# Kernel tuning notes

Measured on AMD Instinct MI355X. Metric: run time of the kernel, lower is better.

Reference implementation:

```python
import jax, jax.numpy as jnp
import numpy as np

B, S, D, H = 4, 2048, 1024, 16
DQKV = max(1, D // H)  # 64


def setup_inputs() -> dict:
    key = jax.random.key(0)
    ks = jax.random.split(key, 12)
    std = 1.0 / np.sqrt(D)
    inp = {
        "query": jax.random.normal(ks[0], (B, S, D), dtype=jnp.float32),
        "key": jax.random.normal(ks[1], (B, S, D), dtype=jnp.float32),
        "value": jax.random.normal(ks[2], (B, S, D), dtype=jnp.float32),
        # per-head projection weights, stacked over heads: [H, DQKV, D] (torch Linear layout [out,in])
        "wq": jax.random.uniform(ks[3], (H, DQKV, D), jnp.float32, -std, std),
        "bq": jax.random.uniform(ks[4], (H, DQKV), jnp.float32, -std, std),
        "wk": jax.random.uniform(ks[5], (H, DQKV, D), jnp.float32, -std, std),
        "bk": jax.random.uniform(ks[6], (H, DQKV), jnp.float32, -std, std),
        "wv": jax.random.uniform(ks[7], (H, DQKV, D), jnp.float32, -std, std),
        "bv": jax.random.uniform(ks[8], (H, DQKV), jnp.float32, -std, std),
        # output projection: [D, H*DQKV]
        "wo": jax.random.uniform(ks[9], (D, H * DQKV), jnp.float32, -1.0 / np.sqrt(H * DQKV), 1.0 / np.sqrt(H * DQKV)),
        "bo": jax.random.uniform(ks[10], (D,), jnp.float32, -1.0 / np.sqrt(H * DQKV), 1.0 / np.sqrt(H * DQKV)),
    }
    return inp


def reference(query, key, value, wq, bq, wk, bk, wv, bv, wo, bo):
    # Per-head linear projections (batched over heads): [B, H, S, DQKV]
    Q = jnp.einsum("bsd,hed->bhse", query, wq) + bq[None, :, None, :]
    K = jnp.einsum("bsd,hed->bhse", key, wk) + bk[None, :, None, :]
    V = jnp.einsum("bsd,hed->bhse", value, wv) + bv[None, :, None, :]
    scale = jnp.asarray(DQKV, Q.dtype) ** 0.5
    # Full N x N attention scores per head (matches naive bmm+softmax+bmm)
    scores = jnp.einsum("bhse,bhte->bhst", Q, K) / scale
    attn = jax.nn.softmax(scores, axis=-1)
    ctx = jnp.einsum("bhst,bhte->bhse", attn, V)  # [B, H, S, DQKV]
    # Concat over heads in head-major order: [B, S, H*DQKV]
    concat = jnp.transpose(ctx, (0, 2, 1, 3)).reshape(ctx.shape[0], ctx.shape[2], H * DQKV)
    return jnp.einsum("bsf,df->bsd", concat, wo) + bo
```

## Files before the change

### kernel.cpp

```cpp
#include <hip/hip_runtime.h>
#include <stdint.h>
#include <stddef.h>


typedef __attribute__((ext_vector_type(8))) short short8;
typedef __attribute__((ext_vector_type(4))) float f32x4;

#if __has_builtin(__builtin_amdgcn_exp2f)
#define EXP2F __builtin_amdgcn_exp2f
#else
#define EXP2F exp2f
#endif
#if __has_builtin(__builtin_amdgcn_rcpf)
#define RCPF __builtin_amdgcn_rcpf
#else
#define RCPF(x) (1.0f / (x))
#endif

__device__ __forceinline__ uint16_t f2bf(float f) {
  uint32_t u = __builtin_bit_cast(uint32_t, f);
  u += 0x7FFFu + ((u >> 16) & 1u);
  return (uint16_t)(u >> 16);
}

__device__ __forceinline__ void gld16(const void* g, void* l) {
  __builtin_amdgcn_global_load_lds((const __attribute__((address_space(1))) void*)g,
                                   (__attribute__((address_space(3))) void*)l, 16, 0, 0);
}

__global__ __launch_bounds__(256) void cast3(const float* __restrict__ s0, const float* __restrict__ s1,
                                             const float* __restrict__ s2, uint16_t* __restrict__ d0,
                                             uint16_t* __restrict__ d1, uint16_t* __restrict__ d2,
                                             int n4) {
  const int z = blockIdx.y;
  const float* s = z == 0 ? s0 : (z == 1 ? s1 : s2);
  uint16_t* d = z == 0 ? d0 : (z == 1 ? d1 : d2);
  int i = blockIdx.x * 256 + threadIdx.x;
  if (i >= n4) return;
  float4 v = ((const float4*)s)[i];
  ushort4 o;
  o.x = f2bf(v.x); o.y = f2bf(v.y); o.z = f2bf(v.z); o.w = f2bf(v.w);
  ((ushort4*)d)[i] = o;
}

__global__ __launch_bounds__(256) void cast4(const float* __restrict__ s0, const float* __restrict__ s1,
                                             const float* __restrict__ s2, const float* __restrict__ s3,
                                             uint16_t* __restrict__ d0, uint16_t* __restrict__ d1,
                                             uint16_t* __restrict__ d2, uint16_t* __restrict__ d3,
                                             int n4) {
  const int z = blockIdx.y;
  const float* s = z == 0 ? s0 : (z == 1 ? s1 : (z == 2 ? s2 : s3));
  uint16_t* d = z == 0 ? d0 : (z == 1 ? d1 : (z == 2 ? d2 : d3));
  int i = blockIdx.x * 256 + threadIdx.x;
  if (i >= n4) return;
  float4 v = ((const float4*)s)[i];
  ushort4 o;
  o.x = f2bf(v.x); o.y = f2bf(v.y); o.z = f2bf(v.z); o.w = f2bf(v.w);
  ((ushort4*)d)[i] = o;
}

__device__ __forceinline__ void gemm_core(const uint16_t* __restrict__ A,
                                          const uint16_t* __restrict__ Bw,
                                          uint16_t* As, uint16_t* Bs,
                                          f32x4 acc[4][4], int m0, int n0) {
  constexpr int K = 1024;
  const int tid = threadIdx.x;
  const int w = tid >> 6, l = tid & 63;
  const int ln = l & 15, quad = l >> 4;
  const int wm = (w >> 1) * 64, wn = (w & 1) * 64;

  const uint16_t* Ag[2];
  const uint16_t* Bg[2];
  int lofs[2];
#pragma unroll
  for (int c = 0; c < 2; ++c) {
    int chunk = w * 128 + c * 64 + l;
    int r = chunk >> 2, cc = chunk & 3;
    Ag[c] = A + (size_t)(m0 + r) * K + cc * 8;
    Bg[c] = Bw + (size_t)(n0 + r) * K + cc * 8;
    lofs[c] = (w * 128 + c * 64) * 8;
  }

  for (int k0 = 0; k0 < K; k0 += 32) {
    __syncthreads();
#pragma unroll
    for (int c = 0; c < 2; ++c) {
      gld16(Ag[c] + k0, As + lofs[c]);
      gld16(Bg[c] + k0, Bs + lofs[c]);
    }
    __syncthreads();
    short8 a[4], b[4];
#pragma unroll
    for (int mt = 0; mt < 4; ++mt)
      a[mt] = *(const short8*)(As + (wm + mt * 16 + ln) * 32 + quad * 8);
#pragma unroll
    for (int nt = 0; nt < 4; ++nt)
      b[nt] = *(const short8*)(Bs + (wn + nt * 16 + ln) * 32 + quad * 8);
#pragma unroll
    for (int mt = 0; mt < 4; ++mt)
#pragma unroll
      for (int nt = 0; nt < 4; ++nt)
        acc[mt][nt] = __builtin_amdgcn_mfma_f32_16x16x32_bf16(a[mt], b[nt], acc[mt][nt], 0, 0, 0);
  }
}

__global__ __launch_bounds__(256) void gemm_qkv(const uint16_t* __restrict__ Xq, const uint16_t* __restrict__ Xk,
                                                const uint16_t* __restrict__ Xv, const uint16_t* __restrict__ Wq,
                                                const uint16_t* __restrict__ Wk, const uint16_t* __restrict__ Wv,
                                                const float* __restrict__ bq, const float* __restrict__ bk,
                                                const float* __restrict__ bv, uint16_t* __restrict__ Qb,
                                                uint16_t* __restrict__ Kb, uint16_t* __restrict__ Vtb,
                                                float qscale, int zbase) {
  __shared__ __attribute__((aligned(16))) uint16_t As[128 * 32];
  __shared__ __attribute__((aligned(16))) uint16_t Bs[128 * 32];
  const int z = blockIdx.z + zbase;
  const uint16_t* A = z == 0 ? Xq : (z == 1 ? Xk : Xv);
  const uint16_t* Bw = z == 0 ? Wq : (z == 1 ? Wk : Wv);
  const float* bias = z == 0 ? bq : (z == 1 ? bk : bv);
  uint16_t* Cout = z == 0 ? Qb : (z == 1 ? Kb : Vtb);
  const float scale = z == 0 ? qscale : 1.0f;

  const int m0 = blockIdx.y * 128, n0 = blockIdx.x * 128;
  f32x4 acc[4][4] = {};
  gemm_core(A, Bw, As, Bs, acc, m0, n0);

  const int tid = threadIdx.x;
  const int w = tid >> 6, l = tid & 63;
  const int ln = l & 15, quad = l >> 4;
  const int wm = (w >> 1) * 64, wn = (w & 1) * 64;
#pragma unroll
  for (int nt = 0; nt < 4; ++nt) {
    const int col = n0 + wn + nt * 16 + ln;
    const float bv_ = bias[col];
    const int h = col >> 6, e = col & 63;
#pragma unroll
    for (int mt = 0; mt < 4; ++mt) {
#pragma unroll
      for (int i = 0; i < 4; ++i) {
        const int row = m0 + wm + mt * 16 + quad * 4 + i;
        const int b_ = row >> 11, s = row & 2047;
        const float v = (acc[mt][nt][i] + bv_) * scale;
        if (z != 2) {
          Cout[(size_t)(b_ * 16 + h) * 131072 + s * 64 + e] = f2bf(v);
        } else {
          Cout[(size_t)(b_ * 16 + h) * 131072 + e * 2048 + s] = f2bf(v);
        }
      }
    }
  }
}

__global__ __launch_bounds__(256) void gemm_out(const uint16_t* __restrict__ A, const uint16_t* __restrict__ Bw,
                                                const float* __restrict__ bias, float* __restrict__ Cout) {
  __shared__ __attribute__((aligned(16))) uint16_t As[128 * 32];
  __shared__ __attribute__((aligned(16))) uint16_t Bs[128 * 32];
  const int m0 = blockIdx.y * 128, n0 = blockIdx.x * 128;
  f32x4 acc[4][4] = {};
  gemm_core(A, Bw, As, Bs, acc, m0, n0);

  const int tid = threadIdx.x;
  const int w = tid >> 6, l = tid & 63;
  const int ln = l & 15, quad = l >> 4;
  const int wm = (w >> 1) * 64, wn = (w & 1) * 64;
#pragma unroll
  for (int nt = 0; nt < 4; ++nt) {
    const int col = n0 + wn + nt * 16 + ln;
    const float bv_ = bias[col];
#pragma unroll
    for (int mt = 0; mt < 4; ++mt)
#pragma unroll
      for (int i = 0; i < 4; ++i) {
        const int row = m0 + wm + mt * 16 + quad * 4 + i;
        Cout[(size_t)row * 1024 + col] = acc[mt][nt][i] + bv_;
      }
  }
}

__global__ __launch_bounds__(256, 4) void attn(const uint16_t* __restrict__ Qb,
                                               const uint16_t* __restrict__ Kb,
                                               const uint16_t* __restrict__ Vtb,
                                               uint16_t* __restrict__ Ctx) {
  __shared__ __attribute__((aligned(16))) uint16_t Ks[64 * 64];
  __shared__ __attribute__((aligned(16))) uint16_t Vs[64 * 64];
  __shared__ __attribute__((aligned(16))) uint16_t Ps[4 * 2 * 16 * 72];
  const int tid = threadIdx.x;
  const int w = tid >> 6, l = tid & 63;
  const int ln = l & 15, quad = l >> 4;
  const int lin = blockIdx.x + (blockIdx.y << 4);
  const int slot = lin >> 3;
  const int bh = (lin & 7) * 8 + (slot >> 4);
  const int q0 = (slot & 15) * 128;
  const int b = bh >> 4, h = bh & 15;
  const uint16_t* Qh = Qb + (size_t)bh * 131072;
  const uint16_t* Kh = Kb + (size_t)bh * 131072;
  const uint16_t* Vth = Vtb + (size_t)bh * 131072;

  short8 qf[2][2];
#pragma unroll
  for (int sub = 0; sub < 2; ++sub)
#pragma unroll
    for (int ks = 0; ks < 2; ++ks)
      qf[sub][ks] = *(const short8*)(Qh + (size_t)(q0 + w * 32 + sub * 16 + ln) * 64 + ks * 32 + quad * 8);

  short8 ones;
#pragma unroll
  for (int j = 0; j < 8; ++j) ones[j] = (short)0x3F80;

  int col[2];
#pragma unroll
  for (int ks = 0; ks < 2; ++ks) col[ks] = (ks * 4 + quad + ln) & 7;
  uint16_t* Pw = Ps + w * 2304;

  f32x4 oacc[2][4] = {};
  f32x4 lacc[2] = {};

  for (int t0 = 0; t0 < 2048; t0 += 64) {
    __syncthreads();
#pragma unroll
    for (int c = 0; c < 2; ++c) {
      const int f = w * 128 + c * 64 + l;
      const int t = f >> 3, g = ((f & 7) - t) & 7;
      gld16(Kh + (size_t)(t0 + t) * 64 + g * 8, Ks + (w * 128 + c * 64) * 8);
      gld16(Vth + (size_t)t * 2048 + t0 + g * 8, Vs + (w * 128 + c * 64) * 8);
    }
    __syncthreads();

    f32x4 sacc[2][4] = {};
    __builtin_amdgcn_s_setprio(1);
#pragma unroll
    for (int nt = 0; nt < 4; ++nt) {
      const int t = nt * 16 + ln;
#pragma unroll
      for (int ks = 0; ks < 2; ++ks) {
        const short8 kf = *(const short8*)(Ks + (t * 8 + col[ks]) * 8);
        sacc[0][nt] = __builtin_amdgcn_mfma_f32_16x16x32_bf16(kf, qf[0][ks], sacc[0][nt], 0, 0, 0);
        sacc[1][nt] = __builtin_amdgcn_mfma_f32_16x16x32_bf16(kf, qf[1][ks], sacc[1][nt], 0, 0, 0);
      }
    }
    __builtin_amdgcn_s_setprio(0);

#pragma unroll
    for (int sub = 0; sub < 2; ++sub)
#pragma unroll
      for (int nt = 0; nt < 4; ++nt) {
        const uint32_t u0 = __builtin_bit_cast(uint32_t, EXP2F(sacc[sub][nt][0]));
        const uint32_t u1 = __builtin_bit_cast(uint32_t, EXP2F(sacc[sub][nt][1]));
        const uint32_t u2 = __builtin_bit_cast(uint32_t, EXP2F(sacc[sub][nt][2]));
        const uint32_t u3 = __builtin_bit_cast(uint32_t, EXP2F(sacc[sub][nt][3]));
        uint2 dd;
        dd.x = ((u0 + 0x7FFFu + ((u0 >> 16) & 1u)) >> 16) |
               ((u1 + 0x7FFFu + ((u1 >> 16) & 1u)) & 0xFFFF0000u);
        dd.y = ((u2 + 0x7FFFu + ((u2 >> 16) & 1u)) >> 16) |
               ((u3 + 0x7FFFu + ((u3 >> 16) & 1u)) & 0xFFFF0000u);
        *(uint2*)(Pw + sub * 1152 + ln * 72 + nt * 16 + quad * 4) = dd;
      }

#pragma unroll
    for (int ks = 0; ks < 2; ++ks) {
      const short8 pf0 = *(const short8*)(Pw + ln * 72 + ks * 32 + quad * 8);
      const short8 pf1 = *(const short8*)(Pw + 1152 + ln * 72 + ks * 32 + quad * 8);
      __builtin_amdgcn_s_setprio(1);
      lacc[0] = __builtin_amdgcn_mfma_f32_16x16x32_bf16(pf0, ones, lacc[0], 0, 0, 0);
      lacc[1] = __builtin_amdgcn_mfma_f32_16x16x32_bf16(pf1, ones, lacc[1], 0, 0, 0);
#pragma unroll
      for (int nt = 0; nt < 4; ++nt) {
        const int e = nt * 16 + ln;
        const short8 vf = *(const short8*)(Vs + (e * 8 + col[ks]) * 8);
        oacc[0][nt] = __builtin_amdgcn_mfma_f32_16x16x32_bf16(pf0, vf, oacc[0][nt], 0, 0, 0);
        oacc[1][nt] = __builtin_amdgcn_mfma_f32_16x16x32_bf16(pf1, vf, oacc[1][nt], 0, 0, 0);
      }
      __builtin_amdgcn_s_setprio(0);
    }
  }

#pragma unroll
  for (int sub = 0; sub < 2; ++sub) {
    float inv[4];
#pragma unroll
    for (int i = 0; i < 4; ++i) inv[i] = RCPF(lacc[sub][i]);
#pragma unroll
    for (int nt = 0; nt < 4; ++nt)
#pragma unroll
      for (int i = 0; i < 4; ++i) {
        const float v = oacc[sub][nt][i] * inv[i];
        const int s = q0 + w * 32 + sub * 16 + quad * 4 + i;
        Ctx[(size_t)(b * 2048 + s) * 1024 + h * 64 + nt * 16 + ln] = f2bf(v);
      }
  }
}

extern "C" void kernel_launch(void* const* d_in, const int* in_sizes, int n_in,
                              void* d_out, int out_size, void* d_ws, size_t ws_size,
                              hipStream_t stream) {
  const float* q = (const float*)d_in[0];
  const float* k = (const float*)d_in[1];
  const float* v = (const float*)d_in[2];
  const float* wq = (const float*)d_in[3];
  const float* bq = (const float*)d_in[4];
  const float* wk = (const float*)d_in[5];
  const float* bk = (const float*)d_in[6];
  const float* wv = (const float*)d_in[7];
  const float* bv = (const float*)d_in[8];
  const float* wo = (const float*)d_in[9];
  const float* bo = (const float*)d_in[10];
  float* out = (float*)d_out;

  uint16_t* ws = (uint16_t*)d_ws;
  uint16_t* Xq = ws;
  uint16_t* Xk = Xq + 8388608;
  uint16_t* Xv = Xk + 8388608;
  uint16_t* Wq = Xv + 8388608;
  uint16_t* Wk = Wq + 1048576;
  uint16_t* Wv = Wk + 1048576;
  uint16_t* Wo = Wv + 1048576;
  uint16_t* Qb = Wo + 1048576;
  uint16_t* Kb = Qb + 8388608;
  uint16_t* Ctx = Xq;

  const size_t fused_elems = 46137344u + 8388608u;
  const bool fused = ws_size >= fused_elems * sizeof(uint16_t);
  uint16_t* Vtb = fused ? (Kb + 8388608) : Xk;

  cast3<<<dim3(8192, 3), 256, 0, stream>>>(q, k, v, Xq, Xk, Xv, 2097152);
  cast4<<<dim3(1024, 4), 256, 0, stream>>>(wq, wk, wv, wo, Wq, Wk, Wv, Wo, 262144);

  const float qscale = 0.125f * 1.4426950408889634f;
  if (fused) {
    gemm_qkv<<<dim3(8, 64, 3), 256, 0, stream>>>(Xq, Xk, Xv, Wq, Wk, Wv, bq, bk, bv,
                                                 Qb, Kb, Vtb, qscale, 0);
  } else {
    gemm_qkv<<<dim3(8, 64, 1), 256, 0, stream>>>(Xq, Xk, Xv, Wq, Wk, Wv, bq, bk, bv,
                                                 Qb, Kb, Vtb, qscale, 0);
    gemm_qkv<<<dim3(8, 64, 1), 256, 0, stream>>>(Xq, Xk, Xv, Wq, Wk, Wv, bq, bk, bv,
                                                 Qb, Kb, Vtb, qscale, 1);
    gemm_qkv<<<dim3(8, 64, 1), 256, 0, stream>>>(Xq, Xk, Xv, Wq, Wk, Wv, bq, bk, bv,
                                                 Qb, Kb, Vtb, qscale, 2);
  }

  attn<<<dim3(16, 64), 256, 0, stream>>>(Qb, Kb, Vtb, Ctx);

  gemm_out<<<dim3(8, 64), 256, 0, stream>>>(Ctx, Wo, bo, out);
}
```

Baseline: 369.8 us.

## Double-buffer GEMM LDS tiles and remap blocks for XCD-local L2 reuse

```diff
diff --git a/kernel.cpp b/kernel.cpp
--- a/kernel.cpp
+++ b/kernel.cpp
@@ -59,6 +59,22 @@
   ((ushort4*)d)[i] = o;
 }
 
+__device__ __forceinline__ void gemm_frag_step(const uint16_t* As, const uint16_t* Bs,
+                                               f32x4 acc[4][4], int wm, int wn, int ln, int quad) {
+  short8 a[4], b[4];
+#pragma unroll
+  for (int mt = 0; mt < 4; ++mt)
+    a[mt] = *(const short8*)(As + (wm + mt * 16 + ln) * 32 + quad * 8);
+#pragma unroll
+  for (int nt = 0; nt < 4; ++nt)
+    b[nt] = *(const short8*)(Bs + (wn + nt * 16 + ln) * 32 + quad * 8);
+#pragma unroll
+  for (int mt = 0; mt < 4; ++mt)
+#pragma unroll
+    for (int nt = 0; nt < 4; ++nt)
+      acc[mt][nt] = __builtin_amdgcn_mfma_f32_16x16x32_bf16(a[mt], b[nt], acc[mt][nt], 0, 0, 0);
+}
+
 __device__ __forceinline__ void gemm_core(const uint16_t* __restrict__ A,
                                           const uint16_t* __restrict__ Bw,
                                           uint16_t* As, uint16_t* Bs,
@@ -81,27 +97,26 @@
     lofs[c] = (w * 128 + c * 64) * 8;
   }
 
-  for (int k0 = 0; k0 < K; k0 += 32) {
+#pragma unroll
+  for (int c = 0; c < 2; ++c) {
+    gld16(Ag[c], As + lofs[c]);
+    gld16(Bg[c], Bs + lofs[c]);
+  }
+  __syncthreads();
+
+  int cur = 0;
+  for (int k0 = 0; k0 < K - 32; k0 += 32) {
+    const int nxt = cur ^ 1;
+#pragma unroll
+    for (int c = 0; c < 2; ++c) {
+      gld16(Ag[c] + k0 + 32, As + nxt * 4096 + lofs[c]);
+      gld16(Bg[c] + k0 + 32, Bs + nxt * 4096 + lofs[c]);
+    }
+    gemm_frag_step(As + cur * 4096, Bs + cur * 4096, acc, wm, wn, ln, quad);
     __syncthreads();
-#pragma unroll
-    for (int c = 0; c < 2; ++c) {
-      gld16(Ag[c] + k0, As + lofs[c]);
-      gld16(Bg[c] + k0, Bs + lofs[c]);
-    }
-    __syncthreads();
-    short8 a[4], b[4];
-#pragma unroll
-    for (int mt = 0; mt < 4; ++mt)
-      a[mt] = *(const short8*)(As + (wm + mt * 16 + ln) * 32 + quad * 8);
-#pragma unroll
-    for (int nt = 0; nt < 4; ++nt)
-      b[nt] = *(const short8*)(Bs + (wn + nt * 16 + ln) * 32 + quad * 8);
-#pragma unroll
-    for (int mt = 0; mt < 4; ++mt)
-#pragma unroll
-      for (int nt = 0; nt < 4; ++nt)
-        acc[mt][nt] = __builtin_amdgcn_mfma_f32_16x16x32_bf16(a[mt], b[nt], acc[mt][nt], 0, 0, 0);
-  }
+    cur = nxt;
+  }
+  gemm_frag_step(As + cur * 4096, Bs + cur * 4096, acc, wm, wn, ln, quad);
 }
 
 __global__ __launch_bounds__(256) void gemm_qkv(const uint16_t* __restrict__ Xq, const uint16_t* __restrict__ Xk,
@@ -111,16 +126,21 @@
                                                 const float* __restrict__ bv, uint16_t* __restrict__ Qb,
                                                 uint16_t* __restrict__ Kb, uint16_t* __restrict__ Vtb,
                                                 float qscale, int zbase) {
-  __shared__ __attribute__((aligned(16))) uint16_t As[128 * 32];
-  __shared__ __attribute__((aligned(16))) uint16_t Bs[128 * 32];
-  const int z = blockIdx.z + zbase;
+  __shared__ __attribute__((aligned(16))) uint16_t As[2 * 128 * 32];
+  __shared__ __attribute__((aligned(16))) uint16_t Bs[2 * 128 * 32];
+  const int lin = blockIdx.x + (blockIdx.y << 3) + (blockIdx.z << 9);
+  const int per = gridDim.z << 3;
+  const int xcd = lin & 7, local = lin >> 3;
+  const int mz = xcd * per + (local >> 3);
+  const int z = (mz >> 6) + zbase;
+  const int m0 = (mz & 63) * 128, n0 = (local & 7) * 128;
+
   const uint16_t* A = z == 0 ? Xq : (z == 1 ? Xk : Xv);
   const uint16_t* Bw = z == 0 ? Wq : (z == 1 ? Wk : Wv);
   const float* bias = z == 0 ? bq : (z == 1 ? bk : bv);
   uint16_t* Cout = z == 0 ? Qb : (z == 1 ? Kb : Vtb);
   const float scale = z == 0 ? qscale : 1.0f;
 
-  const int m0 = blockIdx.y * 128, n0 = blockIdx.x * 128;
   f32x4 acc[4][4] = {};
   gemm_core(A, Bw, As, Bs, acc, m0, n0);
 
@@ -152,9 +172,11 @@
 
 __global__ __launch_bounds__(256) void gemm_out(const uint16_t* __restrict__ A, const uint16_t* __restrict__ Bw,
                                                 const float* __restrict__ bias, float* __restrict__ Cout) {
-  __shared__ __attribute__((aligned(16))) uint16_t As[128 * 32];
-  __shared__ __attribute__((aligned(16))) uint16_t Bs[128 * 32];
-  const int m0 = blockIdx.y * 128, n0 = blockIdx.x * 128;
+  __shared__ __attribute__((aligned(16))) uint16_t As[2 * 128 * 32];
+  __shared__ __attribute__((aligned(16))) uint16_t Bs[2 * 128 * 32];
+  const int lin = blockIdx.x + (blockIdx.y << 3);
+  const int xcd = lin & 7, local = lin >> 3;
+  const int m0 = (xcd * 8 + (local >> 3)) * 128, n0 = (local & 7) * 128;
   f32x4 acc[4][4] = {};
   gemm_core(A, Bw, As, Bs, acc, m0, n0);
 
```

New measurement: 392.9 us. 6.2% more time.

## Widen GEMM K-tile to 64 with swizzled LDS and XCD-aware block remap

Applied to the files above, without the earlier changes.

```diff
diff --git a/kernel.cpp b/kernel.cpp
--- a/kernel.cpp
+++ b/kernel.cpp
@@ -69,38 +69,44 @@
   const int ln = l & 15, quad = l >> 4;
   const int wm = (w >> 1) * 64, wn = (w & 1) * 64;
 
-  const uint16_t* Ag[2];
-  const uint16_t* Bg[2];
-  int lofs[2];
-#pragma unroll
-  for (int c = 0; c < 2; ++c) {
-    int chunk = w * 128 + c * 64 + l;
-    int r = chunk >> 2, cc = chunk & 3;
-    Ag[c] = A + (size_t)(m0 + r) * K + cc * 8;
-    Bg[c] = Bw + (size_t)(n0 + r) * K + cc * 8;
-    lofs[c] = (w * 128 + c * 64) * 8;
-  }
-
-  for (int k0 = 0; k0 < K; k0 += 32) {
+  const uint16_t* Ag[4];
+  const uint16_t* Bg[4];
+  int lofs[4];
+#pragma unroll
+  for (int c = 0; c < 4; ++c) {
+    const int f = c * 256 + tid;
+    const int row = f >> 3, cp = f & 7, g = (cp - row) & 7;
+    Ag[c] = A + (size_t)(m0 + row) * K + g * 8;
+    Bg[c] = Bw + (size_t)(n0 + row) * K + g * 8;
+    lofs[c] = f * 8;
+  }
+  int colk[2];
+#pragma unroll
+  for (int kk = 0; kk < 2; ++kk) colk[kk] = (kk * 4 + quad + ln) & 7;
+
+  for (int k0 = 0; k0 < K; k0 += 64) {
     __syncthreads();
 #pragma unroll
-    for (int c = 0; c < 2; ++c) {
+    for (int c = 0; c < 4; ++c) {
       gld16(Ag[c] + k0, As + lofs[c]);
       gld16(Bg[c] + k0, Bs + lofs[c]);
     }
     __syncthreads();
-    short8 a[4], b[4];
-#pragma unroll
-    for (int mt = 0; mt < 4; ++mt)
-      a[mt] = *(const short8*)(As + (wm + mt * 16 + ln) * 32 + quad * 8);
-#pragma unroll
-    for (int nt = 0; nt < 4; ++nt)
-      b[nt] = *(const short8*)(Bs + (wn + nt * 16 + ln) * 32 + quad * 8);
-#pragma unroll
-    for (int mt = 0; mt < 4; ++mt)
+#pragma unroll
+    for (int kk = 0; kk < 2; ++kk) {
+      short8 a[4], b[4];
+#pragma unroll
+      for (int mt = 0; mt < 4; ++mt)
+        a[mt] = *(const short8*)(As + (wm + mt * 16 + ln) * 64 + colk[kk] * 8);
 #pragma unroll
       for (int nt = 0; nt < 4; ++nt)
-        acc[mt][nt] = __builtin_amdgcn_mfma_f32_16x16x32_bf16(a[mt], b[nt], acc[mt][nt], 0, 0, 0);
+        b[nt] = *(const short8*)(Bs + (wn + nt * 16 + ln) * 64 + colk[kk] * 8);
+#pragma unroll
+      for (int mt = 0; mt < 4; ++mt)
+#pragma unroll
+        for (int nt = 0; nt < 4; ++nt)
+          acc[mt][nt] = __builtin_amdgcn_mfma_f32_16x16x32_bf16(a[mt], b[nt], acc[mt][nt], 0, 0, 0);
+    }
   }
 }
 
@@ -111,16 +117,21 @@
                                                 const float* __restrict__ bv, uint16_t* __restrict__ Qb,
                                                 uint16_t* __restrict__ Kb, uint16_t* __restrict__ Vtb,
                                                 float qscale, int zbase) {
-  __shared__ __attribute__((aligned(16))) uint16_t As[128 * 32];
-  __shared__ __attribute__((aligned(16))) uint16_t Bs[128 * 32];
-  const int z = blockIdx.z + zbase;
+  __shared__ __attribute__((aligned(16))) uint16_t As[128 * 64];
+  __shared__ __attribute__((aligned(16))) uint16_t Bs[128 * 64];
+  const int lin = blockIdx.x + (blockIdx.y << 3) + (blockIdx.z << 9);
+  const int per = gridDim.z << 3;
+  const int xcd = lin & 7, local = lin >> 3;
+  const int mz = xcd * per + (local >> 3);
+  const int z = (mz >> 6) + zbase;
+  const int m0 = (mz & 63) * 128, n0 = (local & 7) * 128;
+
   const uint16_t* A = z == 0 ? Xq : (z == 1 ? Xk : Xv);
   const uint16_t* Bw = z == 0 ? Wq : (z == 1 ? Wk : Wv);
   const float* bias = z == 0 ? bq : (z == 1 ? bk : bv);
   uint16_t* Cout = z == 0 ? Qb : (z == 1 ? Kb : Vtb);
   const float scale = z == 0 ? qscale : 1.0f;
 
-  const int m0 = blockIdx.y * 128, n0 = blockIdx.x * 128;
   f32x4 acc[4][4] = {};
   gemm_core(A, Bw, As, Bs, acc, m0, n0);
 
@@ -152,9 +163,11 @@
 
 __global__ __launch_bounds__(256) void gemm_out(const uint16_t* __restrict__ A, const uint16_t* __restrict__ Bw,
                                                 const float* __restrict__ bias, float* __restrict__ Cout) {
-  __shared__ __attribute__((aligned(16))) uint16_t As[128 * 32];
-  __shared__ __attribute__((aligned(16))) uint16_t Bs[128 * 32];
-  const int m0 = blockIdx.y * 128, n0 = blockIdx.x * 128;
+  __shared__ __attribute__((aligned(16))) uint16_t As[128 * 64];
+  __shared__ __attribute__((aligned(16))) uint16_t Bs[128 * 64];
+  const int lin = blockIdx.x + (blockIdx.y << 3);
+  const int xcd = lin & 7, local = lin >> 3;
+  const int m0 = (xcd * 8 + (local >> 3)) * 128, n0 = (local & 7) * 128;
   f32x4 acc[4][4] = {};
   gemm_core(A, Bw, As, Bs, acc, m0, n0);
 
```

Result: no change. 367.5 us (-0.6%).
